# Kernel optimization log

Measured on AMD Instinct MI355X. Metric: run time of the kernel, lower is better.

Reference implementation:

```python
import jax, jax.numpy as jnp
import numpy as np

H = 256  # hidden_size


def setup_inputs() -> dict:
    key = jax.random.key(0)
    k1, k2, k3 = jax.random.split(key, 3)
    N, L, V, Emb = 128, 2048, 32000, 256
    X = jax.random.randint(k1, (N, L), 0, V, dtype=jnp.int64)
    E = jax.random.normal(k2, (V, Emb), dtype=jnp.float32) * 0.02
    W_w = jax.random.normal(k3, (4 * H, H + Emb), dtype=jnp.float32) * (1.0 / np.sqrt(H + Emb))
    W_b = jnp.zeros((4 * H,), dtype=jnp.float32)
    return {"X": X, "E": E, "W_w": W_w, "W_b": W_b}


def reference(X, E, W_w, W_b):
    # X: (N, L) int token ids
    N, L = X.shape
    Xe = E[X]                      # (N, L, Emb) embedded sequence
    Xe_t = jnp.swapaxes(Xe, 0, 1)  # (L, N, Emb) scan over time

    def step(carry, x_t):
        H_t, C_t = carry
        hx = jnp.concatenate([H_t, x_t], axis=1)           # (N, H+Emb)
        G = hx @ W_w.T + W_b                               # (N, 4H)
        F_g = jax.nn.sigmoid(G[:, :H])
        # NOTE: original code computes I = sigmoid(G[:, H:2H]) but never uses it
        O_g = jax.nn.sigmoid(G[:, 2 * H:3 * H])
        H_tmp = jnp.tanh(G[:, 3 * H:4 * H])
        # Faithful to source: C_t = F*C + O*H_tmp (uses O, not I)
        C_new = F_g * C_t + O_g * H_tmp
        H_new = O_g * jnp.tanh(C_new)
        return (H_new, C_new), None

    init = (jnp.zeros((N, H), Xe.dtype), jnp.zeros((N, H), Xe.dtype))
    (H_last, _), _ = jax.lax.scan(step, init, Xe_t)
    return H_last
```

## Files before the change

kernel.cpp:

```cpp
#include <hip/hip_runtime.h>
#include <hip/hip_bf16.h>

#define N_B   128
#define L_SEQ 2048
#define H_DIM 256
#define EMB   256
#define G3    768
#define G4    1024
#define WROW  512
#define V_SZ  32000


typedef unsigned short ushort_t;
typedef unsigned int   uint_t;

using f32x4  = __attribute__((ext_vector_type(4))) float;
using bf16x8 = __attribute__((ext_vector_type(8))) short;
using h2_t   = __attribute__((ext_vector_type(2))) _Float16;
using ushort4_t = __attribute__((ext_vector_type(4))) ushort_t;
using u32x4  = __attribute__((ext_vector_type(4))) uint_t;

__device__ __forceinline__ float bf2f(ushort_t u) {
  union { uint_t u; float f; } x; x.u = ((uint_t)u) << 16; return x.f;
}
__device__ __forceinline__ ushort_t f2bf(float f) {
  union { float f; uint_t u; } x; x.f = f;
  return (ushort_t)((x.u + 0x7fffu + ((x.u >> 16) & 1u)) >> 16);
}
__device__ __forceinline__ float rcp_f(float x) {
#if __has_builtin(__builtin_amdgcn_rcpf)
  return __builtin_amdgcn_rcpf(x);
#else
  return 1.0f / x;
#endif
}
__device__ __forceinline__ float clampf(float x, float lo, float hi) {
  return fminf(fmaxf(x, lo), hi);
}
__device__ __forceinline__ float sigmoid_f(float x) {
  x = clampf(x, -30.f, 30.f);
  return rcp_f(1.0f + __expf(-x));
}
__device__ __forceinline__ float tanh_f(float x) {
  x = clampf(x, -15.f, 15.f);
  float e = __expf(-2.0f * x);
  return (1.0f - e) * rcp_f(1.0f + e);
}
__device__ __forceinline__ float fdot2_f(h2_t a, h2_t b, float c) {
#if __has_builtin(__builtin_amdgcn_fdot2)
  return __builtin_amdgcn_fdot2(a, b, c, false);
#else
  return c + (float)a.x * (float)b.x + (float)a.y * (float)b.y;
#endif
}
__device__ __forceinline__ uint_t lane_bcast(uint_t v, int l) {
#if __has_builtin(__builtin_amdgcn_readlane)
  return (uint_t)__builtin_amdgcn_readlane((int)v, l);
#else
  return (uint_t)__shfl((int)v, l, 64);
#endif
}
__device__ __forceinline__ h2_t bfpair_to_h2(uint_t u) {
  union { uint_t u; float f; } lo, hi;
  lo.u = u << 16;
  hi.u = u & 0xffff0000u;
  h2_t r; r.x = (_Float16)lo.f; r.y = (_Float16)hi.f; return r;
}

__device__ __forceinline__ int gmap(int g) { return (g < 256) ? g : g + 256; }

#define FENCE_W32(A) asm volatile("" :                                        \
  "+v"(A[0]),  "+v"(A[1]),  "+v"(A[2]),  "+v"(A[3]),                          \
  "+v"(A[4]),  "+v"(A[5]),  "+v"(A[6]),  "+v"(A[7]),                          \
  "+v"(A[8]),  "+v"(A[9]),  "+v"(A[10]), "+v"(A[11]),                         \
  "+v"(A[12]), "+v"(A[13]), "+v"(A[14]), "+v"(A[15]),                         \
  "+v"(A[16]), "+v"(A[17]), "+v"(A[18]), "+v"(A[19]),                         \
  "+v"(A[20]), "+v"(A[21]), "+v"(A[22]), "+v"(A[23]),                         \
  "+v"(A[24]), "+v"(A[25]), "+v"(A[26]), "+v"(A[27]),                         \
  "+v"(A[28]), "+v"(A[29]), "+v"(A[30]), "+v"(A[31]))

__global__ void dtype_probe(const uint_t* __restrict__ Ed,
                            const uint_t* __restrict__ Xd,
                            const uint_t* __restrict__ Wd,
                            uint_t* __restrict__ flags) {
  if (threadIdx.x != 0 || blockIdx.x != 0) return;
  int saneE = 0, saneW = 0;
  for (int i = 0; i < 256; ++i) {
    uint_t le = Ed[i] & 0xffffu, ee = (le >> 7) & 0xffu;
    if (ee == 0u || (ee >= 90u && ee <= 126u)) saneE++;
    uint_t lw = Wd[i] & 0xffffu, ew = (lw >> 7) & 0xffu;
    if (ew == 0u || (ew >= 90u && ew <= 126u)) saneW++;
  }
  uint_t nz = 0u;
  for (int i = 0; i < 128; ++i) nz |= Xd[2 * i + 1];
  flags[0] = (saneE < 192) ? 1u : 0u;
  flags[1] = (nz == 0u) ? 1u : 0u;
  flags[2] = (saneW < 192) ? 1u : 0u;
}

__global__ __launch_bounds__(256) void eg_gemm(const void* __restrict__ Ein,
                                               const void* __restrict__ Wwin,
                                               const void* __restrict__ Wbin,
                                               _Float16* __restrict__ Eg,
                                               const uint_t* __restrict__ flags) {
  __shared__ __align__(16) ushort_t At[16][264];
  const int tid = threadIdx.x;
  const int v0  = blockIdx.x * 16;
  const uint_t ef32 = flags[0];
  const uint_t wf32 = flags[2];

  if (!ef32) {
    const ushort_t* E = (const ushort_t*)Ein;
#pragma unroll
    for (int i = 0; i < 2; ++i) {
      int idx = tid + i * 256;
      int row = idx >> 5, seg = idx & 31;
      const uint4* src = (const uint4*)(E + (size_t)(v0 + row) * EMB + seg * 8);
      *(uint4*)&At[row][seg * 8] = *src;
    }
  } else {
    const float* Ef = (const float*)Ein;
#pragma unroll
    for (int i = 0; i < 4; ++i) {
      int idx = tid + i * 256;
      int row = idx >> 6, seg = idx & 63;
      float4 v = *(const float4*)(Ef + (size_t)(v0 + row) * EMB + seg * 4);
      ushort4_t s;
      s.x = f2bf(v.x); s.y = f2bf(v.y); s.z = f2bf(v.z); s.w = f2bf(v.w);
      *(ushort4_t*)&At[row][seg * 4] = s;
    }
  }
  __syncthreads();

  const int lane = tid & 63, wv = tid >> 6;
  const int m = lane & 15, q = lane >> 4;

  f32x4 acc[12];
#pragma unroll
  for (int nt = 0; nt < 12; ++nt) acc[nt] = f32x4{0.f, 0.f, 0.f, 0.f};

  if (!wf32) {
    const ushort_t* Ww = (const ushort_t*)Wwin;
#pragma unroll
    for (int kt = 0; kt < 8; ++kt) {
      bf16x8 a = *(const bf16x8*)&At[m][kt * 32 + q * 8];
#pragma unroll
      for (int nt = 0; nt < 12; ++nt) {
        int g  = wv * 192 + nt * 16 + m;
        int gr = gmap(g);
        const bf16x8* bp =
            (const bf16x8*)(Ww + (size_t)gr * WROW + EMB + kt * 32 + q * 8);
        acc[nt] = __builtin_amdgcn_mfma_f32_16x16x32_bf16(a, *bp, acc[nt], 0, 0, 0);
      }
    }
  } else {
    const float* Wf = (const float*)Wwin;
#pragma unroll
    for (int kt = 0; kt < 8; ++kt) {
      bf16x8 a = *(const bf16x8*)&At[m][kt * 32 + q * 8];
#pragma unroll
      for (int nt = 0; nt < 12; ++nt) {
        int g  = wv * 192 + nt * 16 + m;
        int gr = gmap(g);
        const float* wp = Wf + (size_t)gr * WROW + EMB + kt * 32 + q * 8;
        float4 w0 = *(const float4*)(wp);
        float4 w1 = *(const float4*)(wp + 4);
        bf16x8 b;
        b[0] = (short)f2bf(w0.x); b[1] = (short)f2bf(w0.y);
        b[2] = (short)f2bf(w0.z); b[3] = (short)f2bf(w0.w);
        b[4] = (short)f2bf(w1.x); b[5] = (short)f2bf(w1.y);
        b[6] = (short)f2bf(w1.z); b[7] = (short)f2bf(w1.w);
        acc[nt] = __builtin_amdgcn_mfma_f32_16x16x32_bf16(a, b, acc[nt], 0, 0, 0);
      }
    }
  }

#pragma unroll
  for (int nt = 0; nt < 12; ++nt) {
    int g  = wv * 192 + nt * 16 + m;
    int gr = gmap(g);
    float bias = wf32 ? ((const float*)Wbin)[gr] : bf2f(((const ushort_t*)Wbin)[gr]);
#pragma unroll
    for (int j = 0; j < 4; ++j) {
      int v = v0 + q * 4 + j;
      Eg[(size_t)v * G3 + g] = (_Float16)(acc[nt][j] + bias);
    }
  }
}

__global__
__attribute__((amdgpu_flat_work_group_size(1024, 1024), amdgpu_waves_per_eu(4, 4)))
void lstm_rec(const int* __restrict__ Xi,
              const void* __restrict__ Wwin,
              const _Float16* __restrict__ Eg,
              float* __restrict__ out,
              const uint_t* __restrict__ flags) {
  __shared__ uint_t hbuf[2][128];
  __shared__ float  pbuf[3][G3];
  const int tid  = threadIdx.x;
  const int lane = tid & 63;
  const int q4   = tid >> 8;
  const int j    = tid & 255;
  const int n    = blockIdx.x;
  const uint_t wf32 = flags[2];
  const uint_t x64  = flags[1];

  uint_t wF[32], wO[32], wT[32];
  if (!wf32) {
    const ushort_t* Wb16 = (const ushort_t*)Wwin;
    const u32x4* sF = (const u32x4*)(Wb16 + (size_t)(j)       * WROW + q4 * 64);
    const u32x4* sO = (const u32x4*)(Wb16 + (size_t)(512 + j) * WROW + q4 * 64);
    const u32x4* sT = (const u32x4*)(Wb16 + (size_t)(768 + j) * WROW + q4 * 64);
#pragma unroll
    for (int i = 0; i < 8; ++i) {
      u32x4 vF = sF[i], vO = sO[i], vT = sT[i];
#pragma unroll
      for (int cdw = 0; cdw < 4; ++cdw) {
        wF[i * 4 + cdw] = __builtin_bit_cast(uint_t, bfpair_to_h2(vF[cdw]));
        wO[i * 4 + cdw] = __builtin_bit_cast(uint_t, bfpair_to_h2(vO[cdw]));
        wT[i * 4 + cdw] = __builtin_bit_cast(uint_t, bfpair_to_h2(vT[cdw]));
      }
    }
  } else {
    const float* Wf = (const float*)Wwin;
    const float* sF = Wf + (size_t)(j)       * WROW + q4 * 64;
    const float* sO = Wf + (size_t)(512 + j) * WROW + q4 * 64;
    const float* sT = Wf + (size_t)(768 + j) * WROW + q4 * 64;
#pragma unroll
    for (int dd = 0; dd < 32; ++dd) {
      float2 vF = *(const float2*)(sF + 2 * dd);
      float2 vO = *(const float2*)(sO + 2 * dd);
      float2 vT = *(const float2*)(sT + 2 * dd);
      h2_t pF, pO, pT;
      pF.x = (_Float16)vF.x; pF.y = (_Float16)vF.y;
      pO.x = (_Float16)vO.x; pO.y = (_Float16)vO.y;
      pT.x = (_Float16)vT.x; pT.y = (_Float16)vT.y;
      wF[dd] = __builtin_bit_cast(uint_t, pF);
      wO[dd] = __builtin_bit_cast(uint_t, pO);
      wT[dd] = __builtin_bit_cast(uint_t, pT);
    }
  }
  FENCE_W32(wF);
  FENCE_W32(wO);
  FENCE_W32(wT);

  if (tid < 128) hbuf[0][tid] = 0u;

  float c = 0.f, hlast = 0.f;
  const size_t xbase = (size_t)n * L_SEQ;

  float pxF = 0.f, pxO = 0.f, pxT = 0.f;
  if (q4 == 0) {
    int tok0 = x64 ? Xi[xbase * 2] : Xi[xbase];
    if ((uint_t)tok0 >= (uint_t)V_SZ) tok0 = 0;
    const _Float16* e = Eg + (size_t)tok0 * G3 + j;
    pxF = (float)e[0]; pxO = (float)e[256]; pxT = (float)e[512];
  }

  int cur = 0;
  for (int t = 0; t < L_SEQ; ++t) {
    __syncthreads();

    const uint_t hv = hbuf[cur][q4 * 32 + (lane & 31)];

    float nF = 0.f, nO = 0.f, nT = 0.f;
    if (q4 == 0) {
      int tp = (t + 1 < L_SEQ) ? (t + 1) : (L_SEQ - 1);
      int tok = x64 ? Xi[(xbase + tp) * 2] : Xi[xbase + tp];
      if ((uint_t)tok >= (uint_t)V_SZ) tok = 0;
      const _Float16* e = Eg + (size_t)tok * G3 + j;
      nF = (float)e[0]; nO = (float)e[256]; nT = (float)e[512];
    }

    float aF0 = 0.f, aO0 = 0.f, aT0 = 0.f;
    float aF1 = 0.f, aO1 = 0.f, aT1 = 0.f;
#pragma unroll
    for (int d = 0; d < 32; ++d) {
      h2_t hh = __builtin_bit_cast(h2_t, lane_bcast(hv, d));
      h2_t wf = __builtin_bit_cast(h2_t, wF[d]);
      h2_t wo = __builtin_bit_cast(h2_t, wO[d]);
      h2_t wt = __builtin_bit_cast(h2_t, wT[d]);
      if (d & 1) {
        aF1 = fdot2_f(wf, hh, aF1);
        aO1 = fdot2_f(wo, hh, aO1);
        aT1 = fdot2_f(wt, hh, aT1);
      } else {
        aF0 = fdot2_f(wf, hh, aF0);
        aO0 = fdot2_f(wo, hh, aO0);
        aT0 = fdot2_f(wt, hh, aT0);
      }
    }
    float aF = aF0 + aF1, aO = aO0 + aO1, aT = aT0 + aT1;

    if (q4 != 0) {
      pbuf[q4 - 1][j]       = aF;
      pbuf[q4 - 1][256 + j] = aO;
      pbuf[q4 - 1][512 + j] = aT;
    }
    __syncthreads();

    if (q4 == 0) {
      aF += pbuf[0][j]       + pbuf[1][j]       + pbuf[2][j]       + pxF;
      aO += pbuf[0][256 + j] + pbuf[1][256 + j] + pbuf[2][256 + j] + pxO;
      aT += pbuf[0][512 + j] + pbuf[1][512 + j] + pbuf[2][512 + j] + pxT;
      float Fg = sigmoid_f(aF);
      float Og = sigmoid_f(aO);
      float Tg = tanh_f(aT);
      c = Fg * c + Og * Tg;
      float hv2 = Og * tanh_f(c);
      hlast = hv2;
      ((_Float16*)hbuf[cur ^ 1])[j] = (_Float16)hv2;
      pxF = nF; pxO = nO; pxT = nT;
    }
    cur ^= 1;
  }

  if (q4 == 0) out[(size_t)n * H_DIM + j] = hlast;
}

extern "C" void kernel_launch(void* const* d_in, const int* in_sizes, int n_in,
                              void* d_out, int out_size, void* d_ws, size_t ws_size,
                              hipStream_t stream) {
  const void* X  = d_in[0];
  const void* E  = d_in[1];
  const void* Ww = d_in[2];
  const void* Wb = d_in[3];
  for (int i = 0; i < n_in && i < 4; ++i) {
    switch (in_sizes[i]) {
      case N_B * L_SEQ: X  = d_in[i]; break;
      case V_SZ * EMB:  E  = d_in[i]; break;
      case G4 * WROW:   Ww = d_in[i]; break;
      case G4:          Wb = d_in[i]; break;
      default: break;
    }
  }
  float* out = (float*)d_out;

  uint_t*   flags = (uint_t*)d_ws;
  _Float16* Eg    = (_Float16*)((char*)d_ws + 256);

  dtype_probe<<<dim3(1), dim3(64), 0, stream>>>(
      (const uint_t*)E, (const uint_t*)X, (const uint_t*)Ww, flags);
  eg_gemm<<<dim3(V_SZ / 16), dim3(256), 0, stream>>>(E, Ww, Wb, Eg, flags);
  lstm_rec<<<dim3(N_B), dim3(1024), 0, stream>>>((const int*)X, Ww, Eg, out, flags);
}
```

Baseline: 3.059 ms.

## Hold full weight rows per thread in 256-thread LSTM blocks, dropping LDS reduction

Shrinks the recurrent kernel from 1024 threads with a four-way split of the hidden dimension to 256 threads that each keep whole F/O/T weight rows in registers. This removes the partial-sum LDS buffer and the second barrier per timestep, so every thread does its own gate math. In exchange each thread runs a four-times-longer dot-product chain and holds about 384 weight registers, which risks spills and leaves only one wave per SIMD to hide latency.

```diff
diff --git a/kernel.cpp b/kernel.cpp
--- a/kernel.cpp
+++ b/kernel.cpp
@@ -70,14 +70,14 @@
 __device__ __forceinline__ int gmap(int g) { return (g < 256) ? g : g + 256; }
 
 #define FENCE_W32(A) asm volatile("" :                                        \
-  "+v"(A[0]),  "+v"(A[1]),  "+v"(A[2]),  "+v"(A[3]),                          \
-  "+v"(A[4]),  "+v"(A[5]),  "+v"(A[6]),  "+v"(A[7]),                          \
-  "+v"(A[8]),  "+v"(A[9]),  "+v"(A[10]), "+v"(A[11]),                         \
-  "+v"(A[12]), "+v"(A[13]), "+v"(A[14]), "+v"(A[15]),                         \
-  "+v"(A[16]), "+v"(A[17]), "+v"(A[18]), "+v"(A[19]),                         \
-  "+v"(A[20]), "+v"(A[21]), "+v"(A[22]), "+v"(A[23]),                         \
-  "+v"(A[24]), "+v"(A[25]), "+v"(A[26]), "+v"(A[27]),                         \
-  "+v"(A[28]), "+v"(A[29]), "+v"(A[30]), "+v"(A[31]))
+  "+v"((A)[0]),  "+v"((A)[1]),  "+v"((A)[2]),  "+v"((A)[3]),                  \
+  "+v"((A)[4]),  "+v"((A)[5]),  "+v"((A)[6]),  "+v"((A)[7]),                  \
+  "+v"((A)[8]),  "+v"((A)[9]),  "+v"((A)[10]), "+v"((A)[11]),                 \
+  "+v"((A)[12]), "+v"((A)[13]), "+v"((A)[14]), "+v"((A)[15]),                 \
+  "+v"((A)[16]), "+v"((A)[17]), "+v"((A)[18]), "+v"((A)[19]),                 \
+  "+v"((A)[20]), "+v"((A)[21]), "+v"((A)[22]), "+v"((A)[23]),                 \
+  "+v"((A)[24]), "+v"((A)[25]), "+v"((A)[26]), "+v"((A)[27]),                 \
+  "+v"((A)[28]), "+v"((A)[29]), "+v"((A)[30]), "+v"((A)[31]))
 
 __global__ void dtype_probe(const uint_t* __restrict__ Ed,
                             const uint_t* __restrict__ Xd,
@@ -189,45 +189,43 @@
 }
 
 __global__
-__attribute__((amdgpu_flat_work_group_size(1024, 1024), amdgpu_waves_per_eu(4, 4)))
+__attribute__((amdgpu_flat_work_group_size(256, 256), amdgpu_waves_per_eu(1, 1)))
 void lstm_rec(const int* __restrict__ Xi,
               const void* __restrict__ Wwin,
               const _Float16* __restrict__ Eg,
               float* __restrict__ out,
               const uint_t* __restrict__ flags) {
   __shared__ uint_t hbuf[2][128];
-  __shared__ float  pbuf[3][G3];
   const int tid  = threadIdx.x;
   const int lane = tid & 63;
-  const int q4   = tid >> 8;
-  const int j    = tid & 255;
+  const int j    = tid;
   const int n    = blockIdx.x;
   const uint_t wf32 = flags[2];
   const uint_t x64  = flags[1];
 
-  uint_t wF[32], wO[32], wT[32];
+  uint_t wF[128], wO[128], wT[128];
   if (!wf32) {
     const ushort_t* Wb16 = (const ushort_t*)Wwin;
-    const u32x4* sF = (const u32x4*)(Wb16 + (size_t)(j)       * WROW + q4 * 64);
-    const u32x4* sO = (const u32x4*)(Wb16 + (size_t)(512 + j) * WROW + q4 * 64);
-    const u32x4* sT = (const u32x4*)(Wb16 + (size_t)(768 + j) * WROW + q4 * 64);
-#pragma unroll
-    for (int i = 0; i < 8; ++i) {
+    const u32x4* sF = (const u32x4*)(Wb16 + (size_t)(j)       * WROW);
+    const u32x4* sO = (const u32x4*)(Wb16 + (size_t)(512 + j) * WROW);
+    const u32x4* sT = (const u32x4*)(Wb16 + (size_t)(768 + j) * WROW);
+#pragma unroll
+    for (int i = 0; i < 32; ++i) {
       u32x4 vF = sF[i], vO = sO[i], vT = sT[i];
 #pragma unroll
-      for (int cdw = 0; cdw < 4; ++cdw) {
-        wF[i * 4 + cdw] = __builtin_bit_cast(uint_t, bfpair_to_h2(vF[cdw]));
-        wO[i * 4 + cdw] = __builtin_bit_cast(uint_t, bfpair_to_h2(vO[cdw]));
-        wT[i * 4 + cdw] = __builtin_bit_cast(uint_t, bfpair_to_h2(vT[cdw]));
+      for (int c4 = 0; c4 < 4; ++c4) {
+        wF[i * 4 + c4] = __builtin_bit_cast(uint_t, bfpair_to_h2(vF[c4]));
+        wO[i * 4 + c4] = __builtin_bit_cast(uint_t, bfpair_to_h2(vO[c4]));
+        wT[i * 4 + c4] = __builtin_bit_cast(uint_t, bfpair_to_h2(vT[c4]));
       }
     }
   } else {
     const float* Wf = (const float*)Wwin;
-    const float* sF = Wf + (size_t)(j)       * WROW + q4 * 64;
-    const float* sO = Wf + (size_t)(512 + j) * WROW + q4 * 64;
-    const float* sT = Wf + (size_t)(768 + j) * WROW + q4 * 64;
-#pragma unroll
-    for (int dd = 0; dd < 32; ++dd) {
+    const float* sF = Wf + (size_t)(j)       * WROW;
+    const float* sO = Wf + (size_t)(512 + j) * WROW;
+    const float* sT = Wf + (size_t)(768 + j) * WROW;
+#pragma unroll
+    for (int dd = 0; dd < 128; ++dd) {
       float2 vF = *(const float2*)(sF + 2 * dd);
       float2 vO = *(const float2*)(sO + 2 * dd);
       float2 vT = *(const float2*)(sT + 2 * dd);
@@ -240,17 +238,17 @@
       wT[dd] = __builtin_bit_cast(uint_t, pT);
     }
   }
-  FENCE_W32(wF);
-  FENCE_W32(wO);
-  FENCE_W32(wT);
+  FENCE_W32(wF);      FENCE_W32(wF + 32); FENCE_W32(wF + 64); FENCE_W32(wF + 96);
+  FENCE_W32(wO);      FENCE_W32(wO + 32); FENCE_W32(wO + 64); FENCE_W32(wO + 96);
+  FENCE_W32(wT);      FENCE_W32(wT + 32); FENCE_W32(wT + 64); FENCE_W32(wT + 96);
 
   if (tid < 128) hbuf[0][tid] = 0u;
 
   float c = 0.f, hlast = 0.f;
   const size_t xbase = (size_t)n * L_SEQ;
 
-  float pxF = 0.f, pxO = 0.f, pxT = 0.f;
-  if (q4 == 0) {
+  float pxF, pxO, pxT;
+  {
     int tok0 = x64 ? Xi[xbase * 2] : Xi[xbase];
     if ((uint_t)tok0 >= (uint_t)V_SZ) tok0 = 0;
     const _Float16* e = Eg + (size_t)tok0 * G3 + j;
@@ -261,10 +259,11 @@
   for (int t = 0; t < L_SEQ; ++t) {
     __syncthreads();
 
-    const uint_t hv = hbuf[cur][q4 * 32 + (lane & 31)];
-
-    float nF = 0.f, nO = 0.f, nT = 0.f;
-    if (q4 == 0) {
+    const uint_t hva = hbuf[cur][lane];
+    const uint_t hvb = hbuf[cur][64 + lane];
+
+    float nF, nO, nT;
+    {
       int tp = (t + 1 < L_SEQ) ? (t + 1) : (L_SEQ - 1);
       int tok = x64 ? Xi[(xbase + tp) * 2] : Xi[xbase + tp];
       if ((uint_t)tok >= (uint_t)V_SZ) tok = 0;
@@ -275,8 +274,8 @@
     float aF0 = 0.f, aO0 = 0.f, aT0 = 0.f;
     float aF1 = 0.f, aO1 = 0.f, aT1 = 0.f;
 #pragma unroll
-    for (int d = 0; d < 32; ++d) {
-      h2_t hh = __builtin_bit_cast(h2_t, lane_bcast(hv, d));
+    for (int d = 0; d < 64; ++d) {
+      h2_t hh = __builtin_bit_cast(h2_t, lane_bcast(hva, d));
       h2_t wf = __builtin_bit_cast(h2_t, wF[d]);
       h2_t wo = __builtin_bit_cast(h2_t, wO[d]);
       h2_t wt = __builtin_bit_cast(h2_t, wT[d]);
@@ -290,32 +289,38 @@
         aT0 = fdot2_f(wt, hh, aT0);
       }
     }
-    float aF = aF0 + aF1, aO = aO0 + aO1, aT = aT0 + aT1;
-
-    if (q4 != 0) {
-      pbuf[q4 - 1][j]       = aF;
-      pbuf[q4 - 1][256 + j] = aO;
-      pbuf[q4 - 1][512 + j] = aT;
-    }
-    __syncthreads();
-
-    if (q4 == 0) {
-      aF += pbuf[0][j]       + pbuf[1][j]       + pbuf[2][j]       + pxF;
-      aO += pbuf[0][256 + j] + pbuf[1][256 + j] + pbuf[2][256 + j] + pxO;
-      aT += pbuf[0][512 + j] + pbuf[1][512 + j] + pbuf[2][512 + j] + pxT;
-      float Fg = sigmoid_f(aF);
-      float Og = sigmoid_f(aO);
-      float Tg = tanh_f(aT);
-      c = Fg * c + Og * Tg;
-      float hv2 = Og * tanh_f(c);
-      hlast = hv2;
-      ((_Float16*)hbuf[cur ^ 1])[j] = (_Float16)hv2;
-      pxF = nF; pxO = nO; pxT = nT;
-    }
+#pragma unroll
+    for (int d = 0; d < 64; ++d) {
+      h2_t hh = __builtin_bit_cast(h2_t, lane_bcast(hvb, d));
+      h2_t wf = __builtin_bit_cast(h2_t, wF[64 + d]);
+      h2_t wo = __builtin_bit_cast(h2_t, wO[64 + d]);
+      h2_t wt = __builtin_bit_cast(h2_t, wT[64 + d]);
+      if (d & 1) {
+        aF1 = fdot2_f(wf, hh, aF1);
+        aO1 = fdot2_f(wo, hh, aO1);
+        aT1 = fdot2_f(wt, hh, aT1);
+      } else {
+        aF0 = fdot2_f(wf, hh, aF0);
+        aO0 = fdot2_f(wo, hh, aO0);
+        aT0 = fdot2_f(wt, hh, aT0);
+      }
+    }
+    float aF = aF0 + aF1 + pxF;
+    float aO = aO0 + aO1 + pxO;
+    float aT = aT0 + aT1 + pxT;
+
+    float Fg = sigmoid_f(aF);
+    float Og = sigmoid_f(aO);
+    float Tg = tanh_f(aT);
+    c = Fg * c + Og * Tg;
+    float hv2 = Og * tanh_f(c);
+    hlast = hv2;
+    ((_Float16*)hbuf[cur ^ 1])[j] = (_Float16)hv2;
+    pxF = nF; pxO = nO; pxT = nT;
     cur ^= 1;
   }
 
-  if (q4 == 0) out[(size_t)n * H_DIM + j] = hlast;
+  out[(size_t)n * H_DIM + j] = hlast;
 }
 
 extern "C" void kernel_launch(void* const* d_in, const int* in_sizes, int n_in,
@@ -342,5 +347,5 @@
   dtype_probe<<<dim3(1), dim3(64), 0, stream>>>(
       (const uint_t*)E, (const uint_t*)X, (const uint_t*)Ww, flags);
   eg_gemm<<<dim3(V_SZ / 16), dim3(256), 0, stream>>>(E, Ww, Wb, Eg, flags);
-  lstm_rec<<<dim3(N_B), dim3(1024), 0, stream>>>((const int*)X, Ww, Eg, out, flags);
-}
+  lstm_rec<<<dim3(N_B), dim3(256), 0, stream>>>((const int*)X, Ww, Eg, out, flags);
+}
```

After: 4.259 ms. 39.3% more time.
